# Optimization experiments

Hardware: AMD Instinct MI355X
Metric: run time of the kernel (lower is better)

The kernel has to match this reference:

```python
import jax, jax.numpy as jnp
import numpy as np

B, S, D = 32, 577, 768
H, Dh = 12, 64  # num_attention_heads, attention_head_size = pruned_dim // heads


def setup_inputs() -> dict:
    key = jax.random.key(0)
    ks = jax.random.split(key, 7)
    s = 1.0 / np.sqrt(D)
    return {
        "hidden_states": jax.random.normal(ks[0], (B, S, D), dtype=jnp.float32),
        "Wq": jax.random.normal(ks[1], (D, H * Dh), dtype=jnp.float32) * s,
        "bq": jnp.zeros((H * Dh,), dtype=jnp.float32),
        "Wk": jax.random.normal(ks[2], (D, H * Dh), dtype=jnp.float32) * s,
        "bk": jnp.zeros((H * Dh,), dtype=jnp.float32),
        "Wv": jax.random.normal(ks[3], (D, H * Dh), dtype=jnp.float32) * s,
        "bv": jnp.zeros((H * Dh,), dtype=jnp.float32),
    }


def reference(hidden_states, Wq, bq, Wk, bk, Wv, bv):
    def heads(x):  # [B,S,H*Dh] -> [B,H,S,Dh]
        return x.reshape(B, S, H, Dh).transpose(0, 2, 1, 3)

    q = heads(hidden_states @ Wq + bq)
    k = heads(hidden_states @ Wk + bk)
    v = heads(hidden_states @ Wv + bv)

    scale = 1.0 / np.sqrt(Dh)
    scores = jnp.einsum("bhqd,bhkd->bhqk", q, k) * scale  # [B,H,S,S]
    probs = jax.nn.softmax(scores, axis=-1)  # dropout p=0.0 -> identity
    ctx = jnp.einsum("bhqk,bhkd->bhqd", probs, v)  # [B,H,S,Dh]
    ctx = ctx.transpose(0, 2, 1, 3).reshape(B, S, H * Dh)
    return ctx
```

## Files before the change

### kernel.cpp

```cpp
#include <hip/hip_runtime.h>

#define NB 32
#define SEQ 577
#define SP 640
#define DM 768
#define NH 12
#define DH 64
#define NC 10

typedef __attribute__((ext_vector_type(8))) short bf16x8;
typedef __attribute__((ext_vector_type(4))) short bf16x4;
typedef __attribute__((ext_vector_type(4))) float f32x4;
typedef __attribute__((ext_vector_type(2))) unsigned int u32x2;
typedef __attribute__((ext_vector_type(4))) unsigned int u32x4;
typedef unsigned short u16;

__device__ __forceinline__ u16 f2bf(float f) {
  unsigned int u = __builtin_bit_cast(unsigned int, f);
  u += 0x7fffu + ((u >> 16) & 1u);
  return (u16)(u >> 16);
}

__device__ __forceinline__ unsigned int pack_bf2(float a, float b) {
  unsigned int ua = __builtin_bit_cast(unsigned int, a) + 0x8000u;
  unsigned int ub = __builtin_bit_cast(unsigned int, b) + 0x8000u;
  return __builtin_amdgcn_perm(ub, ua, 0x07060302u);
}

__device__ __forceinline__ void g2l16(const void* g, void* lds) {
  __builtin_amdgcn_global_load_lds(
      (const __attribute__((address_space(1))) void*)g,
      (__attribute__((address_space(3))) void*)lds, 16, 0, 0);
}

__global__ void cvt_x_kernel(const float* __restrict__ X, u16* __restrict__ Xb, int n4) {
  int i = blockIdx.x * 256 + threadIdx.x;
  if (i >= n4) return;
  f32x4 v = *reinterpret_cast<const f32x4*>(X + (size_t)i * 4);
  u32x2 p;
  p[0] = (unsigned)f2bf(v[0]) | ((unsigned)f2bf(v[1]) << 16);
  p[1] = (unsigned)f2bf(v[2]) | ((unsigned)f2bf(v[3]) << 16);
  *reinterpret_cast<u32x2*>(Xb + (size_t)i * 4) = p;
}

__global__ void cvt_w_kernel(const float* __restrict__ Wq, const float* __restrict__ Wk,
                             const float* __restrict__ Wv, u16* __restrict__ Wt) {
  int idx = blockIdx.x * 256 + threadIdx.x;
  int m = blockIdx.y;
  const float* W = (m == 0) ? Wq : (m == 1) ? Wk : Wv;
  int k = idx / DM, n = idx - k * DM;
  Wt[(size_t)m * DM * DM + (size_t)n * DM + k] = f2bf(W[idx]);
}

__global__ __launch_bounds__(256, 3)
void qkv_gemm_kernel(const u16* __restrict__ Xb, const u16* __restrict__ Wt,
                     const float* __restrict__ bq, const float* __restrict__ bk,
                     const float* __restrict__ bv,
                     u16* __restrict__ Qw, u16* __restrict__ Kw, u16* __restrict__ Vw) {
  __shared__ alignas(16) u16 As[3][128 * 32];
  __shared__ alignas(16) u16 Bs[3][128 * 32];

  const int tid = threadIdx.x;
  const int lane = tid & 63;
  const int wid = tid >> 6;
  const int wr = wid >> 1, wc = wid & 1;
  const int l15 = lane & 15, lq = lane >> 4;

  const int flat = (blockIdx.z * 6 + blockIdx.y) * 160 + blockIdx.x;
  const int xcd = flat & 7;
  const int jj = flat >> 3;
  const int xi = jj / 18;
  const int yz = jj - xi * 18;
  const int mt = xi * 8 + xcd;
  const int nt = yz % 6;
  const int qkv = yz / 6;

  const int b = mt / 5;
  const int t0 = (mt - b * 5) * 128;
  const int n0 = nt * 128;

  const u16* Wm = Wt + (size_t)qkv * DM * DM;
  const float* bias = (qkv == 0) ? bq : (qkv == 1) ? bk : bv;

  int tA0 = t0 + wid * 16 + l15;
  int tA1 = t0 + (wid + 4) * 16 + l15;
  int xr0 = b * SEQ + (tA0 < SEQ ? tA0 : SEQ - 1);
  int xr1 = b * SEQ + (tA1 < SEQ ? tA1 : SEQ - 1);
  const u16* gA0 = Xb + (size_t)xr0 * DM + lq * 8;
  const u16* gA1 = Xb + (size_t)xr1 * DM + lq * 8;
  const u16* gB0 = Wm + (size_t)(n0 + wid * 16 + l15) * DM + lq * 8;
  const u16* gB1 = Wm + (size_t)(n0 + (wid + 4) * 16 + l15) * DM + lq * 8;

  f32x4 acc[4][4];
#pragma unroll
  for (int i = 0; i < 4; ++i)
#pragma unroll
    for (int j = 0; j < 4; ++j)
#pragma unroll
      for (int r = 0; r < 4; ++r) acc[i][j][r] = 0.0f;

  auto stage = [&](int buf, int kt) {
    const int k0 = kt * 32;
    g2l16(gA0 + k0, &As[buf][wid * 512]);
    g2l16(gA1 + k0, &As[buf][(wid + 4) * 512]);
    g2l16(gB0 + k0, &Bs[buf][wid * 512]);
    g2l16(gB1 + k0, &Bs[buf][(wid + 4) * 512]);
  };

  const int NT = DM / 32;

  stage(0, 0);
  stage(1, 1);
  asm volatile("s_waitcnt vmcnt(4)" ::: "memory");
  __builtin_amdgcn_s_barrier();

  bf16x8 af[2][4], bfq[2][4];
#pragma unroll
  for (int i = 0; i < 4; ++i)
    af[0][i] = *reinterpret_cast<const bf16x8*>(&As[0][((wr * 4 + i) * 64 + lane) * 8]);
#pragma unroll
  for (int j = 0; j < 4; ++j)
    bfq[0][j] = *reinterpret_cast<const bf16x8*>(&Bs[0][((wc * 4 + j) * 64 + lane) * 8]);

#pragma unroll
  for (int t = 0; t < NT; ++t) {
    if (t + 2 < NT) stage((t + 2) % 3, t + 2);
    if (t < NT - 1) {
      if (t + 2 < NT)
        asm volatile("s_waitcnt vmcnt(4)" ::: "memory");
      else
        asm volatile("s_waitcnt vmcnt(0)" ::: "memory");
      asm volatile("s_waitcnt lgkmcnt(0)" ::: "memory");
      __builtin_amdgcn_s_barrier();
      const int nb = (t + 1) % 3;
      const int ns = (t + 1) & 1;
#pragma unroll
      for (int i = 0; i < 4; ++i)
        af[ns][i] = *reinterpret_cast<const bf16x8*>(&As[nb][((wr * 4 + i) * 64 + lane) * 8]);
#pragma unroll
      for (int j = 0; j < 4; ++j)
        bfq[ns][j] = *reinterpret_cast<const bf16x8*>(&Bs[nb][((wc * 4 + j) * 64 + lane) * 8]);
    }
    const int cs = t & 1;
#pragma unroll
    for (int i = 0; i < 4; ++i)
#pragma unroll
      for (int j = 0; j < 4; ++j)
        acc[i][j] = __builtin_amdgcn_mfma_f32_16x16x32_bf16(af[cs][i], bfq[cs][j], acc[i][j], 0, 0, 0);
  }

  const float sfold = 0.18033688011112042f;
#pragma unroll
  for (int j = 0; j < 4; ++j) {
    int col = n0 + wc * 64 + j * 16 + l15;
    int h = col >> 6;
    int d = col & 63;
    float bb = bias[col];
#pragma unroll
    for (int i = 0; i < 4; ++i) {
      int trow = t0 + wr * 64 + i * 16 + lq * 4;
      if (qkv == 2) {
        float v0 = acc[i][j][0] + bb, v1 = acc[i][j][1] + bb;
        float v2 = acc[i][j][2] + bb, v3 = acc[i][j][3] + bb;
        u32x2 p;
        p[0] = (unsigned)f2bf(v0) | ((unsigned)f2bf(v1) << 16);
        p[1] = (unsigned)f2bf(v2) | ((unsigned)f2bf(v3) << 16);
        size_t o = ((size_t)(b * NH + h) * DH + d) * SP + trow;
        *reinterpret_cast<u32x2*>(Vw + o) = p;
      } else {
        u16* dst = ((qkv == 0) ? Qw : Kw) + ((size_t)(b * NH + h) * SP + trow) * DH + d;
#pragma unroll
        for (int r = 0; r < 4; ++r) {
          float v = acc[i][j][r] + bb;
          if (qkv == 0) v *= sfold;
          dst[r * DH] = f2bf(v);
        }
      }
    }
  }
}

#if __has_builtin(__builtin_amdgcn_mfma_f32_16x16x16bf16_1k)
#define MFMA16(a, b, c) __builtin_amdgcn_mfma_f32_16x16x16bf16_1k(a, b, c, 0, 0, 0)
#define HAVE_MFMA16 1
#elif __has_builtin(__builtin_amdgcn_mfma_f32_16x16x16_bf16)
#define MFMA16(a, b, c) __builtin_amdgcn_mfma_f32_16x16x16_bf16(a, b, c, 0, 0, 0)
#define HAVE_MFMA16 1
#else
#define HAVE_MFMA16 0
#endif

__global__ __launch_bounds__(256)
void attn_kernel(const u16* __restrict__ Qw, const u16* __restrict__ Kw,
                 const u16* __restrict__ Vw, float* __restrict__ out) {
  __shared__ alignas(16) u16 Kc[2][8 * 64 * 8];
  __shared__ alignas(16) u16 Vc[2][16 * 64 * 4];

  const int tid = threadIdx.x;
  const int lane = tid & 63;
  const int wid = tid >> 6;
  const int l15 = lane & 15, lq = lane >> 4;

  const int flat = blockIdx.y * 5 + blockIdx.x;
  const int w = (flat & 7) * 240 + (flat >> 3);
  const int qx = w % 5;
  const int bh = w / 5;
  const int b = bh / NH;
  const int h = bh - b * NH;
  const int q0 = qx * 128 + wid * 32;

  const u16* Qb = Qw + (size_t)bh * SP * DH;
  const u16* Kb = Kw + (size_t)bh * SP * DH;
  const u16* Vb = Vw + (size_t)bh * DH * SP;

  bf16x8 qf[2][2];
#pragma unroll
  for (int qt = 0; qt < 2; ++qt)
#pragma unroll
    for (int hf = 0; hf < 2; ++hf)
      qf[qt][hf] = *reinterpret_cast<const bf16x8*>(
          &Qb[(q0 + qt * 16 + l15) * DH + hf * 32 + lq * 8]);

  const u16* gK = Kb + (size_t)(wid * 16 + l15) * DH + lq * 8;
  const u16* gV = Vb + (size_t)(wid * 16 + l15) * SP + lq * 4;

  float mrow[2] = {-__builtin_inff(), -__builtin_inff()};
  float lrow[2] = {0.0f, 0.0f};
  f32x4 acc[2][4];
#pragma unroll
  for (int qt = 0; qt < 2; ++qt)
#pragma unroll
    for (int dt = 0; dt < 4; ++dt)
#pragma unroll
      for (int r = 0; r < 4; ++r) acc[qt][dt][r] = 0.0f;

  g2l16(gK, &Kc[0][(wid * 2 + 0) * 512]);
  g2l16(gK + 32, &Kc[0][(wid * 2 + 1) * 512]);
  {
    u32x2 v[4];
#pragma unroll
    for (int t = 0; t < 4; ++t)
      v[t] = *reinterpret_cast<const u32x2*>(gV + t * 16);
#pragma unroll
    for (int t = 0; t < 4; ++t)
      *reinterpret_cast<u32x2*>(&Vc[0][((wid * 4 + t) * 64 + lane) * 4]) = v[t];
  }
  __syncthreads();

  for (int c = 0; c < NC; ++c) {
    const int cur = c & 1;
    const int c0 = c * 64;
    u32x2 vn[4];
    if (c + 1 < NC) {
      const u16* gKn = gK + (size_t)(c0 + 64) * DH;
      g2l16(gKn, &Kc[cur ^ 1][(wid * 2 + 0) * 512]);
      g2l16(gKn + 32, &Kc[cur ^ 1][(wid * 2 + 1) * 512]);
#pragma unroll
      for (int t = 0; t < 4; ++t)
        vn[t] = *reinterpret_cast<const u32x2*>(gV + (c0 + 64) + t * 16);
    }

    f32x4 s[2][4];
    __builtin_amdgcn_s_setprio(1);
#pragma unroll
    for (int t = 0; t < 4; ++t) {
      bf16x8 kf0 = *reinterpret_cast<const bf16x8*>(&Kc[cur][((t * 2 + 0) * 64 + lane) * 8]);
      bf16x8 kf1 = *reinterpret_cast<const bf16x8*>(&Kc[cur][((t * 2 + 1) * 64 + lane) * 8]);
#pragma unroll
      for (int qt = 0; qt < 2; ++qt) {
        f32x4 z;
#pragma unroll
        for (int r = 0; r < 4; ++r) z[r] = 0.0f;
        z = __builtin_amdgcn_mfma_f32_16x16x32_bf16(kf0, qf[qt][0], z, 0, 0, 0);
        z = __builtin_amdgcn_mfma_f32_16x16x32_bf16(kf1, qf[qt][1], z, 0, 0, 0);
        s[qt][t] = z;
      }
    }
    __builtin_amdgcn_s_setprio(0);
    if (c0 + 64 > SEQ) {
#pragma unroll
      for (int qt = 0; qt < 2; ++qt)
#pragma unroll
        for (int t = 0; t < 4; ++t)
#pragma unroll
          for (int r = 0; r < 4; ++r) {
            int key = c0 + t * 16 + lq * 4 + r;
            s[qt][t][r] = (key < SEQ) ? s[qt][t][r] : -__builtin_inff();
          }
    }
    float alpha[2];
    unsigned int pku[2][4][2];
#pragma unroll
    for (int qt = 0; qt < 2; ++qt) {
      float mx = s[qt][0][0];
#pragma unroll
      for (int t = 0; t < 4; ++t)
#pragma unroll
        for (int r = 0; r < 4; ++r) mx = fmaxf(mx, s[qt][t][r]);
      mx = fmaxf(mx, __shfl_xor(mx, 16));
      mx = fmaxf(mx, __shfl_xor(mx, 32));
      float mn = fmaxf(mrow[qt], mx);
      alpha[qt] = __builtin_amdgcn_exp2f(mrow[qt] - mn);
      mrow[qt] = mn;
      float sm = 0.0f;
#pragma unroll
      for (int t = 0; t < 4; ++t) {
        float p0 = __builtin_amdgcn_exp2f(s[qt][t][0] - mn);
        float p1 = __builtin_amdgcn_exp2f(s[qt][t][1] - mn);
        float p2 = __builtin_amdgcn_exp2f(s[qt][t][2] - mn);
        float p3 = __builtin_amdgcn_exp2f(s[qt][t][3] - mn);
        sm += (p0 + p1) + (p2 + p3);
        pku[qt][t][0] = pack_bf2(p0, p1);
        pku[qt][t][1] = pack_bf2(p2, p3);
      }
      sm += __shfl_xor(sm, 16);
      sm += __shfl_xor(sm, 32);
      lrow[qt] = lrow[qt] * alpha[qt] + sm;
    }

#if HAVE_MFMA16
    __builtin_amdgcn_s_setprio(1);
#pragma unroll
    for (int dt = 0; dt < 4; ++dt) {
      bf16x4 vf[4];
#pragma unroll
      for (int t = 0; t < 4; ++t)
        vf[t] = *reinterpret_cast<const bf16x4*>(&Vc[cur][((dt * 4 + t) * 64 + lane) * 4]);
#pragma unroll
      for (int qt = 0; qt < 2; ++qt) {
        f32x4 a = acc[qt][dt];
#pragma unroll
        for (int r = 0; r < 4; ++r) a[r] *= alpha[qt];
#pragma unroll
        for (int t = 0; t < 4; ++t) {
          bf16x4 pf = __builtin_bit_cast(bf16x4, u32x2{pku[qt][t][0], pku[qt][t][1]});
          a = MFMA16(vf[t], pf, a);
        }
        acc[qt][dt] = a;
      }
    }
    __builtin_amdgcn_s_setprio(0);
#else
#pragma unroll
    for (int qt = 0; qt < 2; ++qt) {
      unsigned int bfrag[2][4];
#pragma unroll
      for (int hh = 0; hh < 2; ++hh)
#pragma unroll
        for (int w2 = 0; w2 < 4; ++w2) {
          int srcl = l15 + 16 * (2 * (lq & 1) + (w2 >> 1));
          unsigned int lo = (unsigned int)__shfl((int)pku[qt][2 * hh][w2 & 1], srcl);
          unsigned int hi = (unsigned int)__shfl((int)pku[qt][2 * hh + 1][w2 & 1], srcl);
          bfrag[hh][w2] = (lq < 2) ? lo : hi;
        }
#pragma unroll
      for (int dt = 0; dt < 4; ++dt) {
        f32x4 a = acc[qt][dt];
#pragma unroll
        for (int r = 0; r < 4; ++r) a[r] *= alpha[qt];
#pragma unroll
        for (int hh = 0; hh < 2; ++hh) {
          u32x2 w0 = *reinterpret_cast<const u32x2*>(&Vc[cur][((dt * 4 + 2 * hh) * 64 + lane) * 4]);
          u32x2 w1 = *reinterpret_cast<const u32x2*>(&Vc[cur][((dt * 4 + 2 * hh + 1) * 64 + lane) * 4]);
          u32x4 vw = {w0[0], w0[1], w1[0], w1[1]};
          u32x4 pw = {bfrag[hh][0], bfrag[hh][1], bfrag[hh][2], bfrag[hh][3]};
          a = __builtin_amdgcn_mfma_f32_16x16x32_bf16(
              __builtin_bit_cast(bf16x8, vw), __builtin_bit_cast(bf16x8, pw), a, 0, 0, 0);
        }
        acc[qt][dt] = a;
      }
    }
#endif

    if (c + 1 < NC) {
#pragma unroll
      for (int t = 0; t < 4; ++t)
        *reinterpret_cast<u32x2*>(&Vc[cur ^ 1][((wid * 4 + t) * 64 + lane) * 4]) = vn[t];
    }
    __syncthreads();
  }

#pragma unroll
  for (int qt = 0; qt < 2; ++qt) {
    int q = q0 + qt * 16 + l15;
    if (q < SEQ) {
      float rl = 1.0f / lrow[qt];
      float* orow = out + ((size_t)b * SEQ + q) * DM + h * DH;
#pragma unroll
      for (int dt = 0; dt < 4; ++dt) {
        f32x4 v = acc[qt][dt];
#pragma unroll
        for (int r = 0; r < 4; ++r) v[r] *= rl;
        *reinterpret_cast<f32x4*>(&orow[dt * 16 + lq * 4]) = v;
      }
    }
  }
}

extern "C" void kernel_launch(void* const* d_in, const int* in_sizes, int n_in,
                              void* d_out, int out_size, void* d_ws, size_t ws_size,
                              hipStream_t stream) {
  (void)in_sizes; (void)n_in; (void)out_size; (void)ws_size;
  const float* X  = (const float*)d_in[0];
  const float* Wq = (const float*)d_in[1];
  const float* bq = (const float*)d_in[2];
  const float* Wk = (const float*)d_in[3];
  const float* bk = (const float*)d_in[4];
  const float* Wv = (const float*)d_in[5];
  const float* bv = (const float*)d_in[6];
  float* out = (float*)d_out;

  char* ws = (char*)d_ws;
  u16* Xb = (u16*)ws;
  u16* Wt = (u16*)(ws + 28366848);
  u16* Qw = (u16*)(ws + 28366848 + 3538944);
  u16* Kw = Qw + (size_t)NB * NH * SP * DH;
  u16* Vw = Kw + (size_t)NB * NH * SP * DH;

  cvt_x_kernel<<<dim3(13848), 256, 0, stream>>>(X, Xb, 3545088);
  cvt_w_kernel<<<dim3(2304, 3), 256, 0, stream>>>(Wq, Wk, Wv, Wt);
  qkv_gemm_kernel<<<dim3(160, 6, 3), 256, 0, stream>>>(Xb, Wt, bq, bk, bv, Qw, Kw, Vw);
  attn_kernel<<<dim3(5, NB * NH), 256, 0, stream>>>(Qw, Kw, Vw, out);
}
```

Measured before the change: 364.0 us.

## Enlarge QKV GEMM tiles to 256x256 with 8-wave ping-pong schedule

New measurement: 343.6 us. 5.6% less time.

```diff
diff --git a/kernel.cpp b/kernel.cpp
--- a/kernel.cpp
+++ b/kernel.cpp
@@ -52,123 +52,173 @@
   Wt[(size_t)m * DM * DM + (size_t)n * DM + k] = f2bf(W[idx]);
 }
 
-__global__ __launch_bounds__(256, 3)
+__global__ __launch_bounds__(512, 2)
 void qkv_gemm_kernel(const u16* __restrict__ Xb, const u16* __restrict__ Wt,
                      const float* __restrict__ bq, const float* __restrict__ bk,
                      const float* __restrict__ bv,
                      u16* __restrict__ Qw, u16* __restrict__ Kw, u16* __restrict__ Vw) {
-  __shared__ alignas(16) u16 As[3][128 * 32];
-  __shared__ alignas(16) u16 Bs[3][128 * 32];
+  __shared__ alignas(16) u16 As[2][32 * 512];
+  __shared__ alignas(16) u16 Bs[2][32 * 512];
 
   const int tid = threadIdx.x;
   const int lane = tid & 63;
   const int wid = tid >> 6;
-  const int wr = wid >> 1, wc = wid & 1;
+  const int wm = wid >> 2, wn = wid & 3;
   const int l15 = lane & 15, lq = lane >> 4;
 
-  const int flat = (blockIdx.z * 6 + blockIdx.y) * 160 + blockIdx.x;
+  const int flat = (blockIdx.z * 3 + blockIdx.y) * 80 + blockIdx.x;
   const int xcd = flat & 7;
-  const int jj = flat >> 3;
-  const int xi = jj / 18;
-  const int yz = jj - xi * 18;
+  const int j8 = flat >> 3;
+  const int xi = j8 / 9;
+  const int yz = j8 - xi * 9;
   const int mt = xi * 8 + xcd;
-  const int nt = yz % 6;
-  const int qkv = yz / 6;
-
-  const int b = mt / 5;
-  const int t0 = (mt - b * 5) * 128;
-  const int n0 = nt * 128;
+  const int nt = yz % 3;
+  const int qkv = yz / 3;
 
   const u16* Wm = Wt + (size_t)qkv * DM * DM;
   const float* bias = (qkv == 0) ? bq : (qkv == 1) ? bk : bv;
 
-  int tA0 = t0 + wid * 16 + l15;
-  int tA1 = t0 + (wid + 4) * 16 + l15;
-  int xr0 = b * SEQ + (tA0 < SEQ ? tA0 : SEQ - 1);
-  int xr1 = b * SEQ + (tA1 < SEQ ? tA1 : SEQ - 1);
-  const u16* gA0 = Xb + (size_t)xr0 * DM + lq * 8;
-  const u16* gA1 = Xb + (size_t)xr1 * DM + lq * 8;
-  const u16* gB0 = Wm + (size_t)(n0 + wid * 16 + l15) * DM + lq * 8;
-  const u16* gB1 = Wm + (size_t)(n0 + (wid + 4) * 16 + l15) * DM + lq * 8;
-
-  f32x4 acc[4][4];
-#pragma unroll
-  for (int i = 0; i < 4; ++i)
+  const u16* gA[4];
+  const u16* gB[4];
+#pragma unroll
+  for (int s = 0; s < 4; ++s) {
+    const int e = wid * 4 + s;
+    const int ti = e >> 1, hh = e & 1;
+    int r = mt * 256 + ti * 16 + l15;
+    int br = r / SP;
+    int tr = r - br * SP;
+    if (tr >= SEQ) tr = SEQ - 1;
+    gA[s] = Xb + (size_t)(br * SEQ + tr) * DM + hh * 32 + lq * 8;
+    gB[s] = Wm + (size_t)(nt * 256 + ti * 16 + l15) * DM + hh * 32 + lq * 8;
+  }
+
+  f32x4 acc[8][4];
+#pragma unroll
+  for (int i = 0; i < 8; ++i)
 #pragma unroll
     for (int j = 0; j < 4; ++j)
 #pragma unroll
       for (int r = 0; r < 4; ++r) acc[i][j][r] = 0.0f;
 
-  auto stage = [&](int buf, int kt) {
-    const int k0 = kt * 32;
-    g2l16(gA0 + k0, &As[buf][wid * 512]);
-    g2l16(gA1 + k0, &As[buf][(wid + 4) * 512]);
-    g2l16(gB0 + k0, &Bs[buf][wid * 512]);
-    g2l16(gB1 + k0, &Bs[buf][(wid + 4) * 512]);
+  auto stageA = [&](int buf, int kt) {
+#pragma unroll
+    for (int s = 0; s < 4; ++s)
+      g2l16(gA[s] + kt * 64, &As[buf][(wid * 4 + s) * 512]);
   };
-
-  const int NT = DM / 32;
-
-  stage(0, 0);
-  stage(1, 1);
-  asm volatile("s_waitcnt vmcnt(4)" ::: "memory");
+  auto stageB = [&](int buf, int kt) {
+#pragma unroll
+    for (int s = 0; s < 4; ++s)
+      g2l16(gB[s] + kt * 64, &Bs[buf][(wid * 4 + s) * 512]);
+  };
+
+  stageA(0, 0);
+  stageB(0, 0);
+  asm volatile("s_waitcnt vmcnt(0)" ::: "memory");
   __builtin_amdgcn_s_barrier();
 
-  bf16x8 af[2][4], bfq[2][4];
-#pragma unroll
-  for (int i = 0; i < 4; ++i)
-    af[0][i] = *reinterpret_cast<const bf16x8*>(&As[0][((wr * 4 + i) * 64 + lane) * 8]);
-#pragma unroll
-  for (int j = 0; j < 4; ++j)
-    bfq[0][j] = *reinterpret_cast<const bf16x8*>(&Bs[0][((wc * 4 + j) * 64 + lane) * 8]);
-
-#pragma unroll
-  for (int t = 0; t < NT; ++t) {
-    if (t + 2 < NT) stage((t + 2) % 3, t + 2);
-    if (t < NT - 1) {
-      if (t + 2 < NT)
-        asm volatile("s_waitcnt vmcnt(4)" ::: "memory");
-      else
-        asm volatile("s_waitcnt vmcnt(0)" ::: "memory");
-      asm volatile("s_waitcnt lgkmcnt(0)" ::: "memory");
-      __builtin_amdgcn_s_barrier();
-      const int nb = (t + 1) % 3;
-      const int ns = (t + 1) & 1;
-#pragma unroll
-      for (int i = 0; i < 4; ++i)
-        af[ns][i] = *reinterpret_cast<const bf16x8*>(&As[nb][((wr * 4 + i) * 64 + lane) * 8]);
-#pragma unroll
-      for (int j = 0; j < 4; ++j)
-        bfq[ns][j] = *reinterpret_cast<const bf16x8*>(&Bs[nb][((wc * 4 + j) * 64 + lane) * 8]);
-    }
-    const int cs = t & 1;
-#pragma unroll
-    for (int i = 0; i < 4; ++i)
-#pragma unroll
-      for (int j = 0; j < 4; ++j)
-        acc[i][j] = __builtin_amdgcn_mfma_f32_16x16x32_bf16(af[cs][i], bfq[cs][j], acc[i][j], 0, 0, 0);
+  const int NKT = DM / 64;
+  for (int kt = 0; kt < NKT; ++kt) {
+    const int buf = kt & 1;
+    const bool more = (kt + 1 < NKT);
+    bf16x8 af[4][2], bfr[4][2];
+
+#pragma unroll
+    for (int i = 0; i < 4; ++i)
+#pragma unroll
+      for (int h = 0; h < 2; ++h)
+        af[i][h] = *reinterpret_cast<const bf16x8*>(
+            &As[buf][(((wm * 8 + i) * 2 + h) * 64 + lane) * 8]);
+#pragma unroll
+    for (int j = 0; j < 2; ++j)
+#pragma unroll
+      for (int h = 0; h < 2; ++h)
+        bfr[j][h] = *reinterpret_cast<const bf16x8*>(
+            &Bs[buf][(((wn * 4 + j) * 2 + h) * 64 + lane) * 8]);
+    if (more) stageA(buf ^ 1, kt + 1);
+    __builtin_amdgcn_s_barrier();
+    __builtin_amdgcn_s_setprio(1);
+#pragma unroll
+    for (int i = 0; i < 4; ++i)
+#pragma unroll
+      for (int j = 0; j < 2; ++j)
+#pragma unroll
+        for (int h = 0; h < 2; ++h)
+          acc[i][j] = __builtin_amdgcn_mfma_f32_16x16x32_bf16(af[i][h], bfr[j][h], acc[i][j], 0, 0, 0);
+    __builtin_amdgcn_s_setprio(0);
+    __builtin_amdgcn_s_barrier();
+
+#pragma unroll
+    for (int j = 2; j < 4; ++j)
+#pragma unroll
+      for (int h = 0; h < 2; ++h)
+        bfr[j][h] = *reinterpret_cast<const bf16x8*>(
+            &Bs[buf][(((wn * 4 + j) * 2 + h) * 64 + lane) * 8]);
+    if (more) stageB(buf ^ 1, kt + 1);
+    __builtin_amdgcn_s_barrier();
+    __builtin_amdgcn_s_setprio(1);
+#pragma unroll
+    for (int i = 0; i < 4; ++i)
+#pragma unroll
+      for (int j = 2; j < 4; ++j)
+#pragma unroll
+        for (int h = 0; h < 2; ++h)
+          acc[i][j] = __builtin_amdgcn_mfma_f32_16x16x32_bf16(af[i][h], bfr[j][h], acc[i][j], 0, 0, 0);
+    __builtin_amdgcn_s_setprio(0);
+    __builtin_amdgcn_s_barrier();
+
+#pragma unroll
+    for (int i = 0; i < 4; ++i)
+#pragma unroll
+      for (int h = 0; h < 2; ++h)
+        af[i][h] = *reinterpret_cast<const bf16x8*>(
+            &As[buf][(((wm * 8 + 4 + i) * 2 + h) * 64 + lane) * 8]);
+    __builtin_amdgcn_s_barrier();
+    __builtin_amdgcn_s_setprio(1);
+#pragma unroll
+    for (int i = 0; i < 4; ++i)
+#pragma unroll
+      for (int j = 2; j < 4; ++j)
+#pragma unroll
+        for (int h = 0; h < 2; ++h)
+          acc[4 + i][j] = __builtin_amdgcn_mfma_f32_16x16x32_bf16(af[i][h], bfr[j][h], acc[4 + i][j], 0, 0, 0);
+    __builtin_amdgcn_s_setprio(0);
+    __builtin_amdgcn_s_barrier();
+
+    __builtin_amdgcn_s_setprio(1);
+#pragma unroll
+    for (int i = 0; i < 4; ++i)
+#pragma unroll
+      for (int j = 0; j < 2; ++j)
+#pragma unroll
+        for (int h = 0; h < 2; ++h)
+          acc[4 + i][j] = __builtin_amdgcn_mfma_f32_16x16x32_bf16(af[i][h], bfr[j][h], acc[4 + i][j], 0, 0, 0);
+    __builtin_amdgcn_s_setprio(0);
+    asm volatile("s_waitcnt vmcnt(0)" ::: "memory");
+    __builtin_amdgcn_s_barrier();
   }
 
   const float sfold = 0.18033688011112042f;
 #pragma unroll
   for (int j = 0; j < 4; ++j) {
-    int col = n0 + wc * 64 + j * 16 + l15;
-    int h = col >> 6;
-    int d = col & 63;
-    float bb = bias[col];
-#pragma unroll
-    for (int i = 0; i < 4; ++i) {
-      int trow = t0 + wr * 64 + i * 16 + lq * 4;
+    const int col = nt * 256 + wn * 64 + j * 16 + l15;
+    const int h = col >> 6;
+    const int d = col & 63;
+    const float bb = bias[col];
+#pragma unroll
+    for (int i = 0; i < 8; ++i) {
+      const int rg = mt * 256 + wm * 128 + i * 16 + lq * 4;
+      const int br = rg / SP;
+      const int tr = rg - br * SP;
       if (qkv == 2) {
         float v0 = acc[i][j][0] + bb, v1 = acc[i][j][1] + bb;
         float v2 = acc[i][j][2] + bb, v3 = acc[i][j][3] + bb;
         u32x2 p;
         p[0] = (unsigned)f2bf(v0) | ((unsigned)f2bf(v1) << 16);
         p[1] = (unsigned)f2bf(v2) | ((unsigned)f2bf(v3) << 16);
-        size_t o = ((size_t)(b * NH + h) * DH + d) * SP + trow;
+        size_t o = ((size_t)(br * NH + h) * DH + d) * SP + tr;
         *reinterpret_cast<u32x2*>(Vw + o) = p;
       } else {
-        u16* dst = ((qkv == 0) ? Qw : Kw) + ((size_t)(b * NH + h) * SP + trow) * DH + d;
+        u16* dst = ((qkv == 0) ? Qw : Kw) + ((size_t)(br * NH + h) * SP + tr) * DH + d;
 #pragma unroll
         for (int r = 0; r < 4; ++r) {
           float v = acc[i][j][r] + bb;
@@ -419,6 +469,6 @@
 
   cvt_x_kernel<<<dim3(13848), 256, 0, stream>>>(X, Xb, 3545088);
   cvt_w_kernel<<<dim3(2304, 3), 256, 0, stream>>>(Wq, Wk, Wv, Wt);
-  qkv_gemm_kernel<<<dim3(160, 6, 3), 256, 0, stream>>>(Xb, Wt, bq, bk, bv, Qw, Kw, Vw);
+  qkv_gemm_kernel<<<dim3(80, 3, 3), 512, 0, stream>>>(Xb, Wt, bq, bk, bv, Qw, Kw, Vw);
   attn_kernel<<<dim3(5, NB * NH), 256, 0, stream>>>(Qw, Kw, Vw, out);
 }
```
